# Kernel optimization log

Measured on AMD Instinct MI355X. Metric: run time of the kernel, lower is better.

The kernel has to match this reference:

```python
import jax, jax.numpy as jnp
import numpy as np

N1, N2 = 25000, 25000
N = N1 + N2
E = 800000
D1, D2 = 2000, 500
P = 128        # proj_dim
H, C = 4, 32   # heads, hidden_channels (H*C == 128)
NEG_SLOPE = 0.2


def glorot(key, shape):
    fan_in, fan_out = shape[0], shape[-1]
    s = jnp.sqrt(6.0 / (fan_in + fan_out))
    return jax.random.uniform(key, shape, jnp.float32, -s, s)


def setup_inputs() -> dict:
    key = jax.random.key(0)
    ks = jax.random.split(key, 12)
    return {
        "x_mrna": jax.random.normal(ks[0], (N1, D1), jnp.float32),
        "x_mirna": jax.random.normal(ks[1], (N2, D2), jnp.float32),
        "Wp1": glorot(ks[2], (D1, P)),
        "bp1": jnp.zeros((P,), jnp.float32),
        "Wp2": glorot(ks[3], (D2, P)),
        "bp2": jnp.zeros((P,), jnp.float32),
        "Wl": glorot(ks[4], (P, H * C)),   # GATv2 lin_l (source)
        "Wr": glorot(ks[5], (P, H * C)),   # GATv2 lin_r (target)
        "att": glorot(ks[6], (H, C)),       # GATv2 attention vector a
        "b_gat": jnp.zeros((H * C,), jnp.float32),
        "edge_index": jax.random.randint(ks[7], (2, E), 0, N, jnp.int32),
    }


def gatv2_conv(x, edge_index, Wl, Wr, att, b_gat):
    # x: [N, P] -> out: [N, H*C]; PyG GATv2Conv, add_self_loops=False, concat=True
    src, dst = edge_index[0], edge_index[1]
    xl = (x @ Wl).reshape(N, H, C)  # source-side transform
    xr = (x @ Wr).reshape(N, H, C)  # target-side transform
    # per-edge attention logits: a . LeakyReLU(xl[src] + xr[dst])  -> [E, H]
    g = jax.nn.leaky_relu(xl[src] + xr[dst], NEG_SLOPE)
    e = jnp.einsum('ehc,hc->eh', g, att)
    # softmax over incoming edges per destination node, per head
    m = jax.ops.segment_max(e, dst, num_segments=N)          # [N, H]
    ex = jnp.exp(e - m[dst])                                  # [E, H]
    denom = jax.ops.segment_sum(ex, dst, num_segments=N)     # [N, H]
    alpha = ex / (denom[dst] + 1e-16)                         # [E, H]
    msg = alpha[:, :, None] * xl[src]                         # [E, H, C]
    out = jax.ops.segment_sum(msg, dst, num_segments=N)      # [N, H, C]
    return out.reshape(N, H * C) + b_gat


def reference(x_mrna, x_mirna, Wp1, bp1, Wp2, bp2, Wl, Wr, att, b_gat, edge_index):
    # per-omic projection to shared proj_dim, then stack into one node set
    h1 = x_mrna @ Wp1 + bp1
    h2 = x_mirna @ Wp2 + bp2
    x = jnp.concatenate([h1, h2], axis=0)  # [N, P]
    out = gatv2_conv(x, edge_index, Wl, Wr, att, b_gat)
    return jax.nn.elu(out)
```

## Files before the change

### kernel.cpp

```cpp
#include <hip/hip_runtime.h>

#define NN 50000
#define NE 800000
#define PD 128
#define NBLK 196
#define GB1 391
#define M_HALF 25000

typedef __attribute__((ext_vector_type(8))) short bf16x8;
typedef __attribute__((ext_vector_type(4))) float f32x4;

__device__ __forceinline__ float bf2f(unsigned short h) {
  union { unsigned u; float f; } v; v.u = ((unsigned)h) << 16; return v.f;
}
__device__ __forceinline__ unsigned short f2bf(float f) {
  union { float f; unsigned u; } v; v.f = f;
  unsigned r = (v.u + 0x7FFFu + ((v.u >> 16) & 1u)) >> 16;
  return (unsigned short)r;
}
__device__ __forceinline__ unsigned pack2(float a, float b) {
  return (unsigned)f2bf(a) | ((unsigned)f2bf(b) << 16);
}

__global__ __launch_bounds__(256) void wtrans(
    const float* __restrict__ Wp1, const float* __restrict__ Wp2,
    const float* __restrict__ Wl, const float* __restrict__ Wr,
    const float* __restrict__ bp1, const float* __restrict__ bp2,
    unsigned short* __restrict__ Wct1, unsigned short* __restrict__ Wct2,
    float* __restrict__ biasc, int* __restrict__ deg) {
  int b = blockIdx.x, n = threadIdx.x;
  __shared__ float arow[128];
  if (b > 2560) {
    int i = (b - 2561) * 256 + n;
    if (i < NN) deg[i] = 0;
    return;
  }
  const float* W = (n < 128) ? Wl : Wr;
  int nc = n & 127;
  if (b < 2560) {
    int is1 = (b < 2048) ? 1 : 0;
    int k = is1 ? b : (b - 2048);
    int Kv = is1 ? 2000 : 500;
    unsigned short v = 0;
    if (k < Kv) {
      if (n < 128) arow[n] = is1 ? Wp1[k * 128 + n] : Wp2[k * 128 + n];
      __syncthreads();
      float s = 0.f;
      for (int p = 0; p < 128; ++p) s += arow[p] * W[p * 128 + nc];
      v = f2bf(s);
    }
    int ch = k >> 5, kq = (k >> 3) & 3, e = k & 7;
    size_t idx = (size_t)ch * 8192 + (size_t)(n * 4 + (kq ^ ((n >> 1) & 3))) * 8 + e;
    if (is1) Wct1[idx] = v; else Wct2[idx] = v;
  } else {
    float s1 = 0.f, s2 = 0.f;
    for (int p = 0; p < 128; ++p) {
      float w = W[p * 128 + nc];
      s1 += bp1[p] * w;
      s2 += bp2[p] * w;
    }
    biasc[n] = s1;
    biasc[256 + n] = s2;
  }
}

__global__ __launch_bounds__(256) void big_gemm(
    const float* __restrict__ x1, const float* __restrict__ x2,
    const unsigned short* __restrict__ Wct1, const unsigned short* __restrict__ Wct2,
    const float* __restrict__ biasc,
    unsigned short* __restrict__ XLb, float* __restrict__ XR) {
  __shared__ __align__(64) unsigned short lds[2 * 10752];
  int tid = threadIdx.x;
  int wave = tid >> 6, lane = tid & 63;
  int m16 = lane & 15, quad = lane >> 4;

  int inp = (blockIdx.x >= GB1) ? 1 : 0;
  int blk = inp ? (blockIdx.x - GB1) : blockIdx.x;
  const float* A = inp ? x2 : x1;
  const unsigned short* Wct = inp ? Wct2 : Wct1;
  const int K = inp ? 500 : 2000;
  const int nch = inp ? 16 : 63;
  int row0 = blk * 64;

  int ar = tid >> 2, ako = (tid & 3) << 3;
  int arc = row0 + ar;
  bool arow_ok = arc < M_HALF;
  const float* aptr = A + (size_t)(arow_ok ? arc : 0) * K + ako;

  int swz = (quad ^ ((m16 >> 1) & 3)) << 3;
  int boffA[4], boffB[4];
#pragma unroll
  for (int i = 0; i < 4; ++i) boffA[i] = (i * 16 + m16) * 40 + quad * 8;
#pragma unroll
  for (int j = 0; j < 4; ++j) boffB[j] = (wave * 64 + j * 16 + m16) * 32 + swz;

  f32x4 acc[4][4];
#pragma unroll
  for (int i = 0; i < 4; ++i)
#pragma unroll
    for (int j = 0; j < 4; ++j) acc[i][j] = (f32x4){0.f, 0.f, 0.f, 0.f};

  float4 pa0, pa1;

#define GLB(ch, buf)                                                          \
  {                                                                           \
    const unsigned short* wp_ = Wct + (size_t)(ch) * 8192;                    \
    unsigned short* bb_ = lds + (buf) * 10752 + 2560;                         \
    _Pragma("unroll") for (int ii = 0; ii < 4; ++ii) {                        \
      int gb_ = wave * 256 + ii * 64;                                         \
      __builtin_amdgcn_global_load_lds(                                       \
          (const __attribute__((address_space(1))) void*)(wp_ +               \
              (size_t)(gb_ + lane) * 8),                                      \
          (__attribute__((address_space(3))) void*)(bb_ + (size_t)gb_ * 8),   \
          16, 0, 0);                                                          \
    }                                                                         \
  }

#define LOADA(ch)                                                             \
  {                                                                           \
    int k0_ = (ch) * 32;                                                      \
    pa0 = *(const float4*)(aptr + k0_);                                       \
    pa1 = *(const float4*)(aptr + k0_ + 4);                                   \
  }

#define STOREA(buf)                                                           \
  {                                                                           \
    unsigned short* As_ = lds + (buf) * 10752;                                \
    uint4 wA;                                                                 \
    if (arow_ok) {                                                            \
      wA.x = pack2(pa0.x, pa0.y); wA.y = pack2(pa0.z, pa0.w);                 \
      wA.z = pack2(pa1.x, pa1.y); wA.w = pack2(pa1.z, pa1.w);                 \
    } else { wA.x = wA.y = wA.z = wA.w = 0u; }                                \
    *(uint4*)(As_ + ar * 40 + ako) = wA;                                      \
  }

  LOADA(0);
  GLB(0, 0);
  STOREA(0);
  LOADA(1);

  for (int ch = 0; ch < nch; ++ch) {
    int cur = ch & 1;
    asm volatile("s_waitcnt lgkmcnt(0)" ::: "memory");
    __builtin_amdgcn_s_barrier();
    __builtin_amdgcn_sched_barrier(0);
    if (ch + 1 < nch) {
      GLB(ch + 1, cur ^ 1);
      __builtin_amdgcn_sched_barrier(0);
      asm volatile("s_waitcnt vmcnt(6)" ::: "memory");
    } else {
      asm volatile("s_waitcnt vmcnt(0)" ::: "memory");
    }
    __builtin_amdgcn_sched_barrier(0);
    {
      const unsigned short* As_ = lds + cur * 10752;
      const unsigned short* Bs_ = As_ + 2560;
      bf16x8 a[4], b[4];
#pragma unroll
      for (int i = 0; i < 4; ++i) a[i] = *(const bf16x8*)(As_ + boffA[i]);
#pragma unroll
      for (int j = 0; j < 4; ++j) b[j] = *(const bf16x8*)(Bs_ + boffB[j]);
#pragma unroll
      for (int i = 0; i < 4; ++i)
#pragma unroll
        for (int j = 0; j < 4; ++j)
          acc[i][j] =
              __builtin_amdgcn_mfma_f32_16x16x32_bf16(a[i], b[j], acc[i][j], 0, 0, 0);
    }
    if (ch + 1 < nch) {
      STOREA(cur ^ 1);
      if (ch + 2 < nch) LOADA(ch + 2);
    }
  }

  const float* bc = biasc + inp * 256;
#pragma unroll
  for (int i = 0; i < 4; ++i) {
    int rb = row0 + i * 16 + quad * 4;
#pragma unroll
    for (int j = 0; j < 4; ++j) {
      int c = wave * 64 + j * 16 + m16;
      float bv = bc[c];
#pragma unroll
      for (int r = 0; r < 4; ++r) {
        if (rb + r < M_HALF) {
          size_t grow = (size_t)inp * M_HALF + rb + r;
          float v = acc[i][j][r] + bv;
          if (c < PD) XLb[grow * PD + c] = f2bf(v);
          else XR[grow * PD + (c - PD)] = v;
        }
      }
    }
  }
#undef GLB
#undef LOADA
#undef STOREA
}

__global__ __launch_bounds__(256) void hist(const int* __restrict__ edge,
                                            int* __restrict__ deg) {
  int i = blockIdx.x * 256 + threadIdx.x;
  if (i < NE) atomicAdd(&deg[edge[NE + i]], 1);
}

__global__ __launch_bounds__(256) void scan1(const int* __restrict__ deg,
                                             int* __restrict__ bsum) {
  __shared__ int sd[256];
  int i = blockIdx.x * 256 + threadIdx.x;
  sd[threadIdx.x] = (i < NN) ? deg[i] : 0;
  __syncthreads();
  for (int off = 128; off > 0; off >>= 1) {
    if (threadIdx.x < off) sd[threadIdx.x] += sd[threadIdx.x + off];
    __syncthreads();
  }
  if (threadIdx.x == 0) bsum[blockIdx.x] = sd[0];
}

__global__ __launch_bounds__(256) void scan3(const int* __restrict__ deg,
                                             const int* __restrict__ bsum,
                                             int* __restrict__ start,
                                             int* __restrict__ cursor) {
  __shared__ int sd[256];
  __shared__ int sb[256];
  int t = threadIdx.x;
  int i = blockIdx.x * 256 + t;
  sb[t] = (t < blockIdx.x) ? bsum[t] : 0;
  int v = (i < NN) ? deg[i] : 0;
  sd[t] = v;
  __syncthreads();
  for (int off = 128; off > 0; off >>= 1) {
    if (t < off) sb[t] += sb[t + off];
    __syncthreads();
  }
  for (int off = 1; off < 256; off <<= 1) {
    int x = (t >= off) ? sd[t - off] : 0;
    __syncthreads();
    sd[t] += x;
    __syncthreads();
  }
  if (i < NN) {
    int excl = sb[0] + sd[t] - v;
    start[i] = excl;
    cursor[i] = excl;
  }
  if (blockIdx.x == 0 && t == 0) start[NN] = NE;
}

__global__ __launch_bounds__(256) void scatter(const int* __restrict__ edge,
                                               int* __restrict__ cursor,
                                               int* __restrict__ esrc) {
  int i = blockIdx.x * 256 + threadIdx.x;
  if (i < NE) {
    int dst = edge[NE + i];
    int pos = atomicAdd(&cursor[dst], 1);
    esrc[pos] = edge[i];
  }
}

__global__ __launch_bounds__(256) void gat_fused(
    const unsigned short* __restrict__ XLb, const float* __restrict__ XR,
    const float* __restrict__ att, const float* __restrict__ bg,
    const int* __restrict__ start, const int* __restrict__ esrc,
    float* __restrict__ out) {
  int wave = threadIdx.x >> 6, lane = threadIdx.x & 63;
  int d = blockIdx.x * 4 + wave;
  int f0 = lane * 2;

  float2 xr = *(const float2*)(XR + (size_t)d * PD + f0);
  float a0c = att[f0], a1c = att[f0 + 1];

  int s = start[d], e_end = start[d + 1];

  float m = -INFINITY, l = 0.f, acc0 = 0.f, acc1 = 0.f;

#define UPD(xlu)                                                              \
  {                                                                           \
    float xl0 = bf2f((unsigned short)((xlu) & 0xFFFFu));                      \
    float xl1 = bf2f((unsigned short)((xlu) >> 16));                          \
    float z0 = xl0 + xr.x, z1 = xl1 + xr.y;                                   \
    float g0 = z0 > 0.f ? z0 : 0.2f * z0;                                     \
    float g1 = z1 > 0.f ? z1 : 0.2f * z1;                                     \
    float t = a0c * g0 + a1c * g1;                                            \
    t += __shfl_xor(t, 1);                                                    \
    t += __shfl_xor(t, 2);                                                    \
    t += __shfl_xor(t, 4);                                                    \
    t += __shfl_xor(t, 8);                                                    \
    float mn = fmaxf(m, t);                                                   \
    float c = __expf(m - mn);                                                 \
    float p = __expf(t - mn);                                                 \
    l = l * c + p;                                                            \
    acc0 = acc0 * c + p * xl0;                                                \
    acc1 = acc1 * c + p * xl1;                                                \
    m = mn;                                                                   \
  }

  int j = s;
  for (; j + 4 <= e_end; j += 4) {
    int s0 = esrc[j], s1 = esrc[j + 1], s2 = esrc[j + 2], s3 = esrc[j + 3];
    unsigned u0 = *(const unsigned*)(XLb + (size_t)s0 * PD + f0);
    unsigned u1 = *(const unsigned*)(XLb + (size_t)s1 * PD + f0);
    unsigned u2 = *(const unsigned*)(XLb + (size_t)s2 * PD + f0);
    unsigned u3 = *(const unsigned*)(XLb + (size_t)s3 * PD + f0);
    UPD(u0); UPD(u1); UPD(u2); UPD(u3);
  }
  for (; j < e_end; ++j) {
    int s0 = esrc[j];
    unsigned u0 = *(const unsigned*)(XLb + (size_t)s0 * PD + f0);
    UPD(u0);
  }
#undef UPD

  float inv = 1.f / (l + 1e-16f);
  float v0 = acc0 * inv + bg[f0];
  float v1 = acc1 * inv + bg[f0 + 1];
  v0 = v0 > 0.f ? v0 : expm1f(v0);
  v1 = v1 > 0.f ? v1 : expm1f(v1);
  *(float2*)(out + (size_t)d * PD + f0) = make_float2(v0, v1);
}

extern "C" void kernel_launch(void* const* d_in, const int* in_sizes, int n_in,
                              void* d_out, int out_size, void* d_ws, size_t ws_size,
                              hipStream_t stream) {
  const float* x1  = (const float*)d_in[0];
  const float* x2  = (const float*)d_in[1];
  const float* Wp1 = (const float*)d_in[2];
  const float* bp1 = (const float*)d_in[3];
  const float* Wp2 = (const float*)d_in[4];
  const float* bp2 = (const float*)d_in[5];
  const float* Wl  = (const float*)d_in[6];
  const float* Wr  = (const float*)d_in[7];
  const float* att = (const float*)d_in[8];
  const float* bg  = (const float*)d_in[9];
  const int*   edge = (const int*)d_in[10];

  char* ws = (char*)d_ws;
  unsigned short* XLb   = (unsigned short*)(ws);
  float*          XR    = (float*)(ws + 12800000);
  int*            esrc  = (int*)(ws + 38400000);
  int*            start = (int*)(ws + 41600000);
  int*            cursor = (int*)(ws + 41800192);
  int*            deg   = (int*)(ws + 42000384);
  int*            bsum  = (int*)(ws + 42200576);
  unsigned short* Wct1  = (unsigned short*)(ws + 42202624);
  unsigned short* Wct2  = (unsigned short*)(ws + 43251200);
  float*          biasc = (float*)(ws + 43513344);

  wtrans<<<2757, 256, 0, stream>>>(Wp1, Wp2, Wl, Wr, bp1, bp2, Wct1, Wct2,
                                   biasc, deg);

  hist<<<(NE + 255) / 256, 256, 0, stream>>>(edge, deg);
  scan1<<<NBLK, 256, 0, stream>>>(deg, bsum);
  scan3<<<NBLK, 256, 0, stream>>>(deg, bsum, start, cursor);
  scatter<<<(NE + 255) / 256, 256, 0, stream>>>(edge, cursor, esrc);

  big_gemm<<<GB1 * 2, 256, 0, stream>>>(x1, x2, Wct1, Wct2, biasc, XLb, XR);

  gat_fused<<<NN / 4, 256, 0, stream>>>(XLb, XR, att, bg, start, esrc,
                                        (float*)d_out);
}
```

Baseline: 531.0 us.

## Pre-convert input features to tiled bf16 before GEMM with async LDS loads

Adds a separate kernel that converts the fp32 input features into a bf16, pre-swizzled, chunk-tiled layout in workspace. A new GEMM variant then streams both A and B tiles with global_load_lds instead of loading fp32 through registers and packing in-loop. The aim is to simplify the GEMM main loop and make A loads asynchronous, at the cost of an extra full read/write pass over the input (about 100MB fp32 read plus 50MB bf16 write). It falls back to the old GEMM if the workspace is too small.

```diff
diff --git a/kernel.cpp b/kernel.cpp
--- a/kernel.cpp
+++ b/kernel.cpp
@@ -4,7 +4,7 @@
 #define NE 800000
 #define PD 128
 #define NBLK 196
-#define GB1 391
+#define GBM 391
 #define M_HALF 25000
 
 typedef __attribute__((ext_vector_type(8))) short bf16x8;
@@ -64,7 +64,150 @@
   }
 }
 
-__global__ __launch_bounds__(256) void big_gemm(
+__global__ __launch_bounds__(256) void aprep(
+    const float* __restrict__ x1, const float* __restrict__ x2,
+    unsigned short* __restrict__ Abf1, unsigned short* __restrict__ Abf2) {
+  int inp = (blockIdx.x >= GBM) ? 1 : 0;
+  int rb = inp ? blockIdx.x - GBM : blockIdx.x;
+  const float* X = inp ? x2 : x1;
+  unsigned short* Abf = inp ? Abf2 : Abf1;
+  const int K = inp ? 500 : 2000;
+  const int nch = inp ? 16 : 63;
+  const int nseg = inp ? 2 : 8;
+  const int kpad = nch * 32;
+  int wave = threadIdx.x >> 6, lane = threadIdx.x & 63;
+  size_t tbase = (size_t)rb * nch * 2048;
+
+  for (int r16 = 0; r16 < 16; ++r16) {
+    int r = wave * 16 + r16;
+    int row = rb * 64 + r;
+    if (row >= M_HALF) continue;
+    int sz = (r >> 1) & 3;
+    const float* xrow = X + (size_t)row * K;
+    for (int seg = 0; seg < nseg; ++seg) {
+      int k0 = seg * 256 + lane * 4;
+      if (k0 + 3 < K) {
+        float4 v = *(const float4*)(xrow + k0);
+        int ch = k0 >> 5, kq = (k0 >> 3) & 3, e = k0 & 7;
+        size_t off = tbase + (size_t)ch * 2048 +
+                     (size_t)(r * 4 + (kq ^ sz)) * 8 + e;
+        *(uint2*)(Abf + off) = make_uint2(pack2(v.x, v.y), pack2(v.z, v.w));
+      } else if (k0 < kpad) {
+        int ch = k0 >> 5, kq = (k0 >> 3) & 3, e = k0 & 7;
+        size_t off = tbase + (size_t)ch * 2048 +
+                     (size_t)(r * 4 + (kq ^ sz)) * 8 + e;
+        *(uint2*)(Abf + off) = make_uint2(0u, 0u);
+      }
+    }
+  }
+}
+
+__global__ __launch_bounds__(256) void big_gemm_p(
+    const unsigned short* __restrict__ Abf1, const unsigned short* __restrict__ Abf2,
+    const unsigned short* __restrict__ Wct1, const unsigned short* __restrict__ Wct2,
+    const float* __restrict__ biasc,
+    unsigned short* __restrict__ XLb, float* __restrict__ XR) {
+  __shared__ __align__(64) unsigned short lds[2 * 10240];
+  int tid = threadIdx.x;
+  int wave = tid >> 6, lane = tid & 63;
+  int m16 = lane & 15, quad = lane >> 4;
+
+  int inp = (blockIdx.x >= GBM) ? 1 : 0;
+  int blk = inp ? blockIdx.x - GBM : blockIdx.x;
+  const unsigned short* Abf = inp ? Abf2 : Abf1;
+  const unsigned short* Wct = inp ? Wct2 : Wct1;
+  const int nch = inp ? 16 : 63;
+  int row0 = blk * 64;
+
+  int swz = (quad ^ ((m16 >> 1) & 3)) << 3;
+  int boffA[4], boffB[4];
+#pragma unroll
+  for (int i = 0; i < 4; ++i) boffA[i] = (i * 16 + m16) * 32 + swz;
+#pragma unroll
+  for (int j = 0; j < 4; ++j) boffB[j] = (wave * 64 + j * 16 + m16) * 32 + swz;
+
+  f32x4 acc[4][4];
+#pragma unroll
+  for (int i = 0; i < 4; ++i)
+#pragma unroll
+    for (int j = 0; j < 4; ++j) acc[i][j] = (f32x4){0.f, 0.f, 0.f, 0.f};
+
+#define GLBA(ch, buf)                                                         \
+  {                                                                           \
+    const unsigned short* ap_ = Abf + ((size_t)blk * nch + (ch)) * 2048;      \
+    __builtin_amdgcn_global_load_lds(                                         \
+        (const __attribute__((address_space(1))) void*)(ap_ + (size_t)tid * 8), \
+        (__attribute__((address_space(3))) void*)(lds + (buf) * 10240 +       \
+                                                  wave * 512),                \
+        16, 0, 0);                                                            \
+  }
+
+#define GLBB(ch, buf)                                                         \
+  {                                                                           \
+    const unsigned short* wp_ = Wct + (size_t)(ch) * 8192;                    \
+    unsigned short* bb_ = lds + (buf) * 10240 + 2048;                         \
+    _Pragma("unroll") for (int ii = 0; ii < 4; ++ii) {                        \
+      int gb_ = wave * 256 + ii * 64;                                         \
+      __builtin_amdgcn_global_load_lds(                                       \
+          (const __attribute__((address_space(1))) void*)(wp_ +               \
+              (size_t)(gb_ + lane) * 8),                                      \
+          (__attribute__((address_space(3))) void*)(bb_ + (size_t)gb_ * 8),   \
+          16, 0, 0);                                                          \
+    }                                                                         \
+  }
+
+  GLBA(0, 0);
+  GLBB(0, 0);
+
+  for (int ch = 0; ch < nch; ++ch) {
+    int cur = ch & 1;
+    asm volatile("s_waitcnt vmcnt(0)" ::: "memory");
+    __builtin_amdgcn_s_barrier();
+    if (ch + 1 < nch) {
+      GLBA(ch + 1, cur ^ 1);
+      GLBB(ch + 1, cur ^ 1);
+    }
+    {
+      const unsigned short* As_ = lds + cur * 10240;
+      const unsigned short* Bs_ = As_ + 2048;
+      bf16x8 a[4], b[4];
+#pragma unroll
+      for (int i = 0; i < 4; ++i) a[i] = *(const bf16x8*)(As_ + boffA[i]);
+#pragma unroll
+      for (int j = 0; j < 4; ++j) b[j] = *(const bf16x8*)(Bs_ + boffB[j]);
+#pragma unroll
+      for (int i = 0; i < 4; ++i)
+#pragma unroll
+        for (int j = 0; j < 4; ++j)
+          acc[i][j] =
+              __builtin_amdgcn_mfma_f32_16x16x32_bf16(a[i], b[j], acc[i][j], 0, 0, 0);
+    }
+  }
+
+  const float* bc = biasc + inp * 256;
+#pragma unroll
+  for (int i = 0; i < 4; ++i) {
+    int rb = row0 + i * 16 + quad * 4;
+#pragma unroll
+    for (int j = 0; j < 4; ++j) {
+      int c = wave * 64 + j * 16 + m16;
+      float bv = bc[c];
+#pragma unroll
+      for (int r = 0; r < 4; ++r) {
+        if (rb + r < M_HALF) {
+          size_t grow = (size_t)inp * M_HALF + rb + r;
+          float v = acc[i][j][r] + bv;
+          if (c < PD) XLb[grow * PD + c] = f2bf(v);
+          else XR[grow * PD + (c - PD)] = v;
+        }
+      }
+    }
+  }
+#undef GLBA
+#undef GLBB
+}
+
+__global__ __launch_bounds__(256) void big_gemm_f(
     const float* __restrict__ x1, const float* __restrict__ x2,
     const unsigned short* __restrict__ Wct1, const unsigned short* __restrict__ Wct2,
     const float* __restrict__ biasc,
@@ -74,8 +217,8 @@
   int wave = tid >> 6, lane = tid & 63;
   int m16 = lane & 15, quad = lane >> 4;
 
-  int inp = (blockIdx.x >= GB1) ? 1 : 0;
-  int blk = inp ? (blockIdx.x - GB1) : blockIdx.x;
+  int inp = (blockIdx.x >= GBM) ? 1 : 0;
+  int blk = inp ? (blockIdx.x - GBM) : blockIdx.x;
   const float* A = inp ? x2 : x1;
   const unsigned short* Wct = inp ? Wct2 : Wct1;
   const int K = inp ? 500 : 2000;
@@ -115,14 +258,12 @@
           16, 0, 0);                                                          \
     }                                                                         \
   }
-
 #define LOADA(ch)                                                             \
   {                                                                           \
     int k0_ = (ch) * 32;                                                      \
     pa0 = *(const float4*)(aptr + k0_);                                       \
     pa1 = *(const float4*)(aptr + k0_ + 4);                                   \
   }
-
 #define STOREA(buf)                                                           \
   {                                                                           \
     unsigned short* As_ = lds + (buf) * 10752;                                \
@@ -344,16 +485,27 @@
   unsigned short* Wct1  = (unsigned short*)(ws + 42202624);
   unsigned short* Wct2  = (unsigned short*)(ws + 43251200);
   float*          biasc = (float*)(ws + 43513344);
+  unsigned short* Abf1  = (unsigned short*)(ws + 43520000);
+  unsigned short* Abf2  = (unsigned short*)(ws + 144416768);
+  const size_t NEED = 170041344 + 64;
+  bool prep = (ws_size >= NEED);
 
   wtrans<<<2757, 256, 0, stream>>>(Wp1, Wp2, Wl, Wr, bp1, bp2, Wct1, Wct2,
                                    biasc, deg);
+
+  if (prep) aprep<<<GBM * 2, 256, 0, stream>>>(x1, x2, Abf1, Abf2);
 
   hist<<<(NE + 255) / 256, 256, 0, stream>>>(edge, deg);
   scan1<<<NBLK, 256, 0, stream>>>(deg, bsum);
   scan3<<<NBLK, 256, 0, stream>>>(deg, bsum, start, cursor);
   scatter<<<(NE + 255) / 256, 256, 0, stream>>>(edge, cursor, esrc);
 
-  big_gemm<<<GB1 * 2, 256, 0, stream>>>(x1, x2, Wct1, Wct2, biasc, XLb, XR);
+  if (prep)
+    big_gemm_p<<<GBM * 2, 256, 0, stream>>>(Abf1, Abf2, Wct1, Wct2, biasc,
+                                            XLb, XR);
+  else
+    big_gemm_f<<<GBM * 2, 256, 0, stream>>>(x1, x2, Wct1, Wct2, biasc,
+                                            XLb, XR);
 
   gat_fused<<<NN / 4, 256, 0, stream>>>(XLb, XR, att, bg, start, esrc,
                                         (float*)d_out);
```

New measurement: 633.0 us. 19.2% more time.

## Deepen GEMM weight prefetch to four LDS stages and unroll gather loop by eight

Applied to the files above, without the earlier changes.

The big GEMM now keeps four LDS buffers for the weight tiles and issues global-to-LDS loads three chunks ahead, with per-iteration vmcnt waits, while the activation tile stays double-buffered. The aim is to hide more of the global load latency behind the MFMA work. The cost is more LDS per block (about 75 KB), which may lower occupancy. Separately, the GAT aggregation loop now unrolls to eight neighbour gathers per iteration, so more memory loads are in flight at once.

```diff
diff --git a/kernel.cpp b/kernel.cpp
--- a/kernel.cpp
+++ b/kernel.cpp
@@ -4,7 +4,7 @@
 #define NE 800000
 #define PD 128
 #define NBLK 196
-#define GB1 391
+#define GBM 391
 #define M_HALF 25000
 
 typedef __attribute__((ext_vector_type(8))) short bf16x8;
@@ -69,13 +69,13 @@
     const unsigned short* __restrict__ Wct1, const unsigned short* __restrict__ Wct2,
     const float* __restrict__ biasc,
     unsigned short* __restrict__ XLb, float* __restrict__ XR) {
-  __shared__ __align__(64) unsigned short lds[2 * 10752];
+  __shared__ __align__(64) unsigned short lds[5120 + 4 * 8192];
   int tid = threadIdx.x;
   int wave = tid >> 6, lane = tid & 63;
   int m16 = lane & 15, quad = lane >> 4;
 
-  int inp = (blockIdx.x >= GB1) ? 1 : 0;
-  int blk = inp ? (blockIdx.x - GB1) : blockIdx.x;
+  int inp = (blockIdx.x >= GBM) ? 1 : 0;
+  int blk = inp ? (blockIdx.x - GBM) : blockIdx.x;
   const float* A = inp ? x2 : x1;
   const unsigned short* Wct = inp ? Wct2 : Wct1;
   const int K = inp ? 500 : 2000;
@@ -102,10 +102,10 @@
 
   float4 pa0, pa1;
 
-#define GLB(ch, buf)                                                          \
+#define GLBB(ch)                                                              \
   {                                                                           \
     const unsigned short* wp_ = Wct + (size_t)(ch) * 8192;                    \
-    unsigned short* bb_ = lds + (buf) * 10752 + 2560;                         \
+    unsigned short* bb_ = lds + 5120 + ((ch) & 3) * 8192;                     \
     _Pragma("unroll") for (int ii = 0; ii < 4; ++ii) {                        \
       int gb_ = wave * 256 + ii * 64;                                         \
       __builtin_amdgcn_global_load_lds(                                       \
@@ -123,9 +123,9 @@
     pa1 = *(const float4*)(aptr + k0_ + 4);                                   \
   }
 
-#define STOREA(buf)                                                           \
+#define STOREA(ch)                                                            \
   {                                                                           \
-    unsigned short* As_ = lds + (buf) * 10752;                                \
+    unsigned short* As_ = lds + ((ch) & 1) * 2560;                            \
     uint4 wA;                                                                 \
     if (arow_ok) {                                                            \
       wA.x = pack2(pa0.x, pa0.y); wA.y = pack2(pa0.z, pa0.w);                 \
@@ -135,26 +135,29 @@
   }
 
   LOADA(0);
-  GLB(0, 0);
+  GLBB(0);
+  GLBB(1);
+  GLBB(2);
   STOREA(0);
   LOADA(1);
 
   for (int ch = 0; ch < nch; ++ch) {
-    int cur = ch & 1;
     asm volatile("s_waitcnt lgkmcnt(0)" ::: "memory");
+    if (ch >= nch - 3) {
+      asm volatile("s_waitcnt vmcnt(0)" ::: "memory");
+    } else if (ch == 0) {
+      asm volatile("s_waitcnt vmcnt(10)" ::: "memory");
+    } else if (ch == 1) {
+      asm volatile("s_waitcnt vmcnt(12)" ::: "memory");
+    } else {
+      asm volatile("s_waitcnt vmcnt(14)" ::: "memory");
+    }
     __builtin_amdgcn_s_barrier();
     __builtin_amdgcn_sched_barrier(0);
-    if (ch + 1 < nch) {
-      GLB(ch + 1, cur ^ 1);
-      __builtin_amdgcn_sched_barrier(0);
-      asm volatile("s_waitcnt vmcnt(6)" ::: "memory");
-    } else {
-      asm volatile("s_waitcnt vmcnt(0)" ::: "memory");
-    }
-    __builtin_amdgcn_sched_barrier(0);
+    if (ch + 3 < nch) GLBB(ch + 3);
     {
-      const unsigned short* As_ = lds + cur * 10752;
-      const unsigned short* Bs_ = As_ + 2560;
+      const unsigned short* As_ = lds + (ch & 1) * 2560;
+      const unsigned short* Bs_ = lds + 5120 + (ch & 3) * 8192;
       bf16x8 a[4], b[4];
 #pragma unroll
       for (int i = 0; i < 4; ++i) a[i] = *(const bf16x8*)(As_ + boffA[i]);
@@ -168,7 +171,7 @@
               __builtin_amdgcn_mfma_f32_16x16x32_bf16(a[i], b[j], acc[i][j], 0, 0, 0);
     }
     if (ch + 1 < nch) {
-      STOREA(cur ^ 1);
+      STOREA(ch + 1);
       if (ch + 2 < nch) LOADA(ch + 2);
     }
   }
@@ -192,7 +195,7 @@
       }
     }
   }
-#undef GLB
+#undef GLBB
 #undef LOADA
 #undef STOREA
 }
@@ -295,13 +298,19 @@
   }
 
   int j = s;
-  for (; j + 4 <= e_end; j += 4) {
-    int s0 = esrc[j], s1 = esrc[j + 1], s2 = esrc[j + 2], s3 = esrc[j + 3];
+  for (; j + 8 <= e_end; j += 8) {
+    int s0 = esrc[j],     s1 = esrc[j + 1], s2 = esrc[j + 2], s3 = esrc[j + 3];
+    int s4 = esrc[j + 4], s5 = esrc[j + 5], s6 = esrc[j + 6], s7 = esrc[j + 7];
     unsigned u0 = *(const unsigned*)(XLb + (size_t)s0 * PD + f0);
     unsigned u1 = *(const unsigned*)(XLb + (size_t)s1 * PD + f0);
     unsigned u2 = *(const unsigned*)(XLb + (size_t)s2 * PD + f0);
     unsigned u3 = *(const unsigned*)(XLb + (size_t)s3 * PD + f0);
+    unsigned u4 = *(const unsigned*)(XLb + (size_t)s4 * PD + f0);
+    unsigned u5 = *(const unsigned*)(XLb + (size_t)s5 * PD + f0);
+    unsigned u6 = *(const unsigned*)(XLb + (size_t)s6 * PD + f0);
+    unsigned u7 = *(const unsigned*)(XLb + (size_t)s7 * PD + f0);
     UPD(u0); UPD(u1); UPD(u2); UPD(u3);
+    UPD(u4); UPD(u5); UPD(u6); UPD(u7);
   }
   for (; j < e_end; ++j) {
     int s0 = esrc[j];
@@ -353,7 +362,7 @@
   scan3<<<NBLK, 256, 0, stream>>>(deg, bsum, start, cursor);
   scatter<<<(NE + 255) / 256, 256, 0, stream>>>(edge, cursor, esrc);
 
-  big_gemm<<<GB1 * 2, 256, 0, stream>>>(x1, x2, Wct1, Wct2, biasc, XLb, XR);
+  big_gemm<<<GBM * 2, 256, 0, stream>>>(x1, x2, Wct1, Wct2, biasc, XLb, XR);
 
   gat_fused<<<NN / 4, 256, 0, stream>>>(XLb, XR, att, bg, start, esrc,
                                         (float*)d_out);
```

New measurement: 548.9 us. 3.4% more time.
